# Kernel tuning notes

Hardware: AMD Instinct MI355X
Metric: run time of the kernel (lower is better)

Reference implementation:

```python
import jax, jax.numpy as jnp
import numpy as np

B, S, HID, H, D = 4, 1024, 1024, 16, 64
MAXP = 1024  # max_position_embeddings
EPS = 1e-8


def setup_inputs() -> dict:
    key = jax.random.key(0)
    ks = jax.random.split(key, 9)
    scale = 0.02  # keep logits small since masked_softmax has no max-subtraction
    return {
        "hidden_states": jax.random.normal(ks[0], (B, S, HID), jnp.float32),
        "attention_mask": jnp.zeros((B, 1, 1, S), jnp.float32),
        "skim_mask": jax.random.randint(ks[1], (B, S), 0, 2, jnp.int32),
        "Wq": jax.random.normal(ks[2], (HID, HID), jnp.float32) * scale,
        "bq": jnp.zeros((HID,), jnp.float32),
        "Wk": jax.random.normal(ks[3], (HID, HID), jnp.float32) * scale,
        "bk": jnp.zeros((HID,), jnp.float32),
        "Wv": jax.random.normal(ks[4], (HID, HID), jnp.float32) * scale,
        "bv": jnp.zeros((HID,), jnp.float32),
        "dist_emb": jax.random.normal(ks[5], (2 * MAXP - 1, D), jnp.float32) * scale,
    }


def reference(hidden_states, attention_mask, skim_mask, Wq, bq, Wk, bk, Wv, bv, dist_emb):
    # Linear projections (W stored as [in, out]) then split heads: [B,H,S,D]
    def heads(x):
        return x.reshape(B, S, H, D).transpose(0, 2, 1, 3)

    q = heads(hidden_states @ Wq + bq)
    k = heads(hidden_states @ Wk + bk)
    v = heads(hidden_states @ Wv + bv)

    # raw scores [B,H,S,S]
    scores = jnp.einsum('bhld,bhrd->bhlr', q, k)

    # relative_key positional bias
    pos = jnp.arange(S)
    distance = pos[:, None] - pos[None, :]                 # [S,S]
    pe = dist_emb[distance + MAXP - 1]                     # [S,S,D]
    scores = scores + jnp.einsum('bhld,lrd->bhlr', q, pe)

    scores = scores / jnp.sqrt(jnp.float32(D))
    scores = scores + attention_mask

    # skim_mask branch: masked_softmax (exp * mask, normalized with eps)
    mask = skim_mask[:, None, None, :].astype(scores.dtype)  # [B,1,1,S]
    exps = jnp.exp(scores) * mask
    probs = exps / (EPS + exps.sum(-1, keepdims=True))
    # dropout in eval mode -> identity

    ctx = jnp.einsum('bhlr,bhrd->bhld', probs, v)
    return ctx.transpose(0, 2, 1, 3).reshape(B, S, HID)
```

## Files before the change

### kernel.cpp

```cpp
#include <hip/hip_runtime.h>
#include <hip/hip_bf16.h>


#define EPSV 1e-8f

typedef short bfrag __attribute__((ext_vector_type(8)));
typedef float cfrag __attribute__((ext_vector_type(16)));

__device__ __forceinline__ short f2bf(float f) {
    __hip_bfloat16 h = __float2bfloat16(f);
    return *reinterpret_cast<short*>(&h);
}
__device__ __forceinline__ float bf2f(short s) {
    unsigned int u = ((unsigned int)(unsigned short)s) << 16;
    return __builtin_bit_cast(float, u);
}
__device__ __forceinline__ unsigned int pk2(short a, short b) {
    return (unsigned int)(unsigned short)a | ((unsigned int)(unsigned short)b << 16);
}

__global__ __launch_bounds__(256) void prep(
    const float* __restrict__ hidden, const float* __restrict__ Wq,
    const float* __restrict__ Wk, const float* __restrict__ Wv,
    const float* __restrict__ dist,
    short* __restrict__ Xs, short* __restrict__ Wt, short* __restrict__ Db)
{
    __shared__ short Tl[32 * 72];
    const int bid = blockIdx.x, tid = threadIdx.x;

    if (bid < 2048) {
        const int mt = bid >> 4, kg = bid & 15;
        const int m_l = tid >> 3, k8 = (tid & 7) * 8;
        const float* src = hidden + (size_t)(mt * 32 + m_l) * 1024 + kg * 64 + k8;
        float4 v0 = *(const float4*)src, v1 = *(const float4*)(src + 4);
        short o[8];
        o[0] = f2bf(v0.x); o[1] = f2bf(v0.y); o[2] = f2bf(v0.z); o[3] = f2bf(v0.w);
        o[4] = f2bf(v1.x); o[5] = f2bf(v1.y); o[6] = f2bf(v1.z); o[7] = f2bf(v1.w);
        *(bfrag*)&Tl[m_l * 72 + k8] = *(bfrag*)o;
        __syncthreads();
        const int l31 = tid & 31, q2 = (tid >> 5) & 1, kc = tid >> 6;
        bfrag r = *(const bfrag*)&Tl[l31 * 72 + kc * 16 + q2 * 8];
        *(bfrag*)(Xs + ((size_t)(mt * 64 + kg * 4 + kc) * 64 + q2 * 32 + l31) * 8) = r;
    } else if (bid < 3584) {
        const int t = bid - 2048, z = t >> 9, nt = (t >> 4) & 31, kg = t & 15;
        const float* W = (z == 0) ? Wq : ((z == 1) ? Wk : Wv);
        const int k_l = tid >> 2, n8 = (tid & 3) * 8;
        const float* src = W + (size_t)(kg * 64 + k_l) * 1024 + nt * 32 + n8;
        float4 v0 = *(const float4*)src, v1 = *(const float4*)(src + 4);
        float vv[8] = {v0.x, v0.y, v0.z, v0.w, v1.x, v1.y, v1.z, v1.w};
#pragma unroll
        for (int i = 0; i < 8; i++)
            Tl[(n8 + i) * 72 + k_l] = f2bf(vv[i]);
        __syncthreads();
        const int l31 = tid & 31, q2 = (tid >> 5) & 1, kc = tid >> 6;
        bfrag r = *(const bfrag*)&Tl[l31 * 72 + kc * 16 + q2 * 8];
        *(bfrag*)(Wt + (size_t)z * 1048576
                  + ((size_t)(nt * 64 + kg * 4 + kc) * 64 + q2 * 32 + l31) * 8) = r;
    } else {
        const int idx = (bid - 3584) * 256 + tid;
        if (idx < 16376) {
            const float* src = dist + (size_t)idx * 8;
            float4 v0 = *(const float4*)src, v1 = *(const float4*)(src + 4);
            short o[8];
            o[0] = f2bf(v0.x); o[1] = f2bf(v0.y); o[2] = f2bf(v0.z); o[3] = f2bf(v0.w);
            o[4] = f2bf(v1.x); o[5] = f2bf(v1.y); o[6] = f2bf(v1.z); o[7] = f2bf(v1.w);
            *(bfrag*)(Db + (size_t)idx * 8) = *(bfrag*)o;
        }
    }
}

__global__ __launch_bounds__(256) void qkv_mfma(
    const short* __restrict__ Xs, const short* __restrict__ Wt,
    const float* __restrict__ bq, const float* __restrict__ bk,
    const float* __restrict__ bv,
    short* __restrict__ Qf, short* __restrict__ Kf, short* __restrict__ Vt)
{
    const int z = blockIdx.z;
    const short* W = Wt + (size_t)z * 1048576;
    const float* bias = (z == 0) ? bq : ((z == 1) ? bk : bv);
    const float scale = (z == 0) ? 0.125f : 1.0f;

    const int tid = threadIdx.x, lane = tid & 63, wid = tid >> 6;
    const int q2 = lane >> 5, l31 = lane & 31;
    const int wr = wid >> 1, wc = wid & 1;
    const int m0 = blockIdx.x * 128, n0 = blockIdx.y * 128;

    cfrag acc[2][2];
#pragma unroll
    for (int i = 0; i < 2; i++)
#pragma unroll
        for (int j = 0; j < 2; j++)
#pragma unroll
            for (int e = 0; e < 16; e++) acc[i][j][e] = 0.f;

    const short* ap0 = Xs + ((size_t)((m0 >> 5) + wr * 2 + 0) * 64 * 64 + lane) * 8;
    const short* ap1 = Xs + ((size_t)((m0 >> 5) + wr * 2 + 1) * 64 * 64 + lane) * 8;
    const short* bp0 = W  + ((size_t)((n0 >> 5) + wc * 2 + 0) * 64 * 64 + lane) * 8;
    const short* bp1 = W  + ((size_t)((n0 >> 5) + wc * 2 + 1) * 64 * 64 + lane) * 8;

#pragma unroll 4
    for (int kc = 0; kc < 64; kc++) {
        const int off = kc * 512;
        bfrag a0 = *(const bfrag*)(ap0 + off);
        bfrag a1 = *(const bfrag*)(ap1 + off);
        bfrag b0 = *(const bfrag*)(bp0 + off);
        bfrag b1 = *(const bfrag*)(bp1 + off);
        acc[0][0] = __builtin_amdgcn_mfma_f32_32x32x16_bf16(a0, b0, acc[0][0], 0, 0, 0);
        acc[0][1] = __builtin_amdgcn_mfma_f32_32x32x16_bf16(a0, b1, acc[0][1], 0, 0, 0);
        acc[1][0] = __builtin_amdgcn_mfma_f32_32x32x16_bf16(a1, b0, acc[1][0], 0, 0, 0);
        acc[1][1] = __builtin_amdgcn_mfma_f32_32x32x16_bf16(a1, b1, acc[1][1], 0, 0, 0);
    }

#pragma unroll
    for (int nt = 0; nt < 2; nt++) {
        const int c = n0 + wc * 64 + nt * 32 + l31;
        const float bval = bias[c];
        const int h = c >> 6;
        const int d = nt * 32 + l31;
#pragma unroll
        for (int mt = 0; mt < 2; mt++) {
            const int tok0 = m0 + wr * 64 + mt * 32;
            const int bb = tok0 >> 10, s_base = tok0 & 1023;
            const size_t bhbase = (size_t)(bb * 16 + h) * 65536;
            if (z < 2) {
                short* outp = (z == 0) ? Qf : Kf;
                const size_t fbase = bhbase
                    + ((size_t)((s_base >> 5) * 4 + (d >> 4)) * 64
                       + ((d >> 3) & 1) * 32) * 8 + (d & 7);
#pragma unroll
                for (int reg = 0; reg < 16; reg++) {
                    const int row = (reg & 3) + 8 * (reg >> 2) + 4 * q2;
                    outp[fbase + (size_t)row * 8] = f2bf((acc[mt][nt][reg] + bval) * scale);
                }
            } else {
#pragma unroll
                for (int g = 0; g < 4; g++) {
                    const float e0 = acc[mt][nt][4 * g + 0] + bval;
                    const float e1 = acc[mt][nt][4 * g + 1] + bval;
                    const float e2 = acc[mt][nt][4 * g + 2] + bval;
                    const float e3 = acc[mt][nt][4 * g + 3] + bval;
                    uint2 w2;
                    w2.x = pk2(f2bf(e0), f2bf(e1));
                    w2.y = pk2(f2bf(e2), f2bf(e3));
                    const size_t flat = bhbase
                        + ((size_t)(nt * 64 + (s_base >> 4) + (g >> 1)) * 64
                           + (g & 1) * 32 + l31) * 8 + 4 * q2;
                    *(uint2*)(Vt + flat) = w2;
                }
            }
        }
    }
}

__global__ __launch_bounds__(256) void attn_mfma(
    const short* __restrict__ Qf, const short* __restrict__ Kf,
    const short* __restrict__ Vt, const short* __restrict__ Db,
    const float* __restrict__ amask, const int* __restrict__ skim,
    float* __restrict__ out)
{
    __shared__ short Tb[128 * 132];
    __shared__ short Es[4][32 * 72];
    __shared__ float Lg[1024];

    const int tid = threadIdx.x, lane = tid & 63, w = tid >> 6;
    const int q2 = lane >> 5, l31 = lane & 31;
    const int h2 = w >> 1;
    const int bh = blockIdx.x, b = bh >> 4, hh = bh & 15;
    const int l0 = blockIdx.y * 128;

    {
        const int r4 = tid * 4;
        float4 am = *(const float4*)(amask + b * 1024 + r4);
        int4 sk = *(const int4*)(skim + b * 1024 + r4);
        Lg[r4 + 0] = __expf(am.x) * (float)sk.x;
        Lg[r4 + 1] = __expf(am.y) * (float)sk.y;
        Lg[r4 + 2] = __expf(am.z) * (float)sk.z;
        Lg[r4 + 3] = __expf(am.w) * (float)sk.w;
    }
    __syncthreads();

    const short* Qg = Qf + (size_t)bh * 65536;
    const short* Kg = Kf + (size_t)bh * 65536;
    const short* Vg = Vt + (size_t)bh * 65536;

    bfrag qa[4];
#pragma unroll
    for (int c = 0; c < 4; c++)
        qa[c] = *(const bfrag*)(Qg + ((size_t)(((l0 >> 5) + w) * 4 + c) * 64 + lane) * 8);

    cfrag oacc[2];
#pragma unroll
    for (int mt = 0; mt < 2; mt++)
#pragma unroll
        for (int e = 0; e < 16; e++) oacc[mt][e] = 0.f;
    float esum = 0.f;

    const int lrow = 32 * w + l31;

    for (int r0 = -64; r0 < 1024; r0 += 64) {
        const int bd = l0 - r0 - 64 + 64 * h2;
#pragma unroll
        for (int mt = 0; mt < 2; mt++) {
            cfrag t;
#pragma unroll
            for (int e = 0; e < 16; e++) t[e] = 0.f;
            const int drow = bd + 32 * mt + l31;
            const int er = min(max(drow + 1023, 0), 2046);
#pragma unroll
            for (int kc = 0; kc < 4; kc++) {
                bfrag pb = *(const bfrag*)(Db + (size_t)er * 64 + kc * 16 + q2 * 8);
                t = __builtin_amdgcn_mfma_f32_32x32x16_bf16(pb, qa[kc], t, 0, 0, 0);
            }
#pragma unroll
            for (int g = 0; g < 4; g++) {
                const int slot = (bd + 32 * mt + 8 * g + 4 * q2) & 127;
                uint2 w2;
                w2.x = pk2(f2bf(t[4 * g + 0]), f2bf(t[4 * g + 1]));
                w2.y = pk2(f2bf(t[4 * g + 2]), f2bf(t[4 * g + 3]));
                *(uint2*)&Tb[lrow * 132 + slot] = w2;
            }
        }
        if (r0 < 0) continue;

        cfrag sfr[2];
#pragma unroll
        for (int mt = 0; mt < 2; mt++) {
#pragma unroll
            for (int e = 0; e < 16; e++) sfr[mt][e] = 0.f;
#pragma unroll
            for (int kc = 0; kc < 4; kc++) {
                bfrag kb = *(const bfrag*)(Kg
                    + ((size_t)(((r0 >> 5) + mt) * 4 + kc) * 64 + lane) * 8);
                sfr[mt] = __builtin_amdgcn_mfma_f32_32x32x16_bf16(
                    kb, qa[kc], sfr[mt], 0, 0, 0);
            }
        }

        const int lg = l0 + 32 * w + l31;
#pragma unroll
        for (int mt = 0; mt < 2; mt++) {
#pragma unroll
            for (int g = 0; g < 4; g++) {
                const int rb = r0 + 32 * mt + 8 * g + 4 * q2;
                float4 g4 = *(const float4*)&Lg[rb];
                short s4[4];
#pragma unroll
                for (int j = 0; j < 4; j++) {
                    const int dist = lg - (rb + j);
                    const float tv = bf2f(Tb[lrow * 132 + (dist & 127)]);
                    const float gv = (j == 0) ? g4.x : (j == 1) ? g4.y
                                   : (j == 2) ? g4.z : g4.w;
                    const float e = __expf(sfr[mt][4 * g + j] + tv) * gv;
                    s4[j] = f2bf(e);
                    esum += bf2f(s4[j]);
                }
                uint2 w2;
                w2.x = pk2(s4[0], s4[1]);
                w2.y = pk2(s4[2], s4[3]);
                *(uint2*)&Es[w][l31 * 72 + 32 * mt + 8 * g + 4 * q2] = w2;
            }
        }

#pragma unroll
        for (int kc = 0; kc < 4; kc++) {
            bfrag ef = *(const bfrag*)&Es[w][l31 * 72 + kc * 16 + q2 * 8];
#pragma unroll
            for (int mtd = 0; mtd < 2; mtd++) {
                bfrag vb = *(const bfrag*)(Vg
                    + ((size_t)(mtd * 64 + (r0 >> 4) + kc) * 64 + lane) * 8);
                oacc[mtd] = __builtin_amdgcn_mfma_f32_32x32x16_bf16(
                    vb, ef, oacc[mtd], 0, 0, 0);
            }
        }
    }

    const float den = EPSV + esum + __shfl_xor(esum, 32);
    const float inv = 1.0f / den;
    const int lg = l0 + 32 * w + l31;
    float* ob = out + ((size_t)(b * 1024 + lg) * 1024) + hh * 64;
#pragma unroll
    for (int mtd = 0; mtd < 2; mtd++) {
#pragma unroll
        for (int g = 0; g < 4; g++) {
            float4 o;
            o.x = oacc[mtd][4 * g + 0] * inv;
            o.y = oacc[mtd][4 * g + 1] * inv;
            o.z = oacc[mtd][4 * g + 2] * inv;
            o.w = oacc[mtd][4 * g + 3] * inv;
            *(float4*)(ob + 32 * mtd + 8 * g + 4 * q2) = o;
        }
    }
}

extern "C" void kernel_launch(void* const* d_in, const int* in_sizes, int n_in,
                              void* d_out, int out_size, void* d_ws, size_t ws_size,
                              hipStream_t stream) {
    const float* hidden = (const float*)d_in[0];
    const float* amask  = (const float*)d_in[1];
    const int*   skim   = (const int*)d_in[2];
    const float* Wq     = (const float*)d_in[3];
    const float* bq     = (const float*)d_in[4];
    const float* Wk     = (const float*)d_in[5];
    const float* bk     = (const float*)d_in[6];
    const float* Wv     = (const float*)d_in[7];
    const float* bv     = (const float*)d_in[8];
    const float* dist   = (const float*)d_in[9];
    float* out = (float*)d_out;

    char* w = (char*)d_ws;
    short* Xs  = (short*)(w);
    short* Wt  = (short*)(w + ((size_t)8 << 20));
    short* Db  = (short*)(w + ((size_t)14 << 20));
    short* Qf  = (short*)(w + ((size_t)15 << 20));
    short* Kf  = (short*)(w + ((size_t)23 << 20));
    short* Vt  = (short*)(w + ((size_t)31 << 20));

    prep<<<3648, 256, 0, stream>>>(hidden, Wq, Wk, Wv, dist, Xs, Wt, Db);
    qkv_mfma<<<dim3(32, 8, 3), 256, 0, stream>>>(Xs, Wt, bq, bk, bv, Qf, Kf, Vt);
    attn_mfma<<<dim3(64, 8), 256, 0, stream>>>(Qf, Kf, Vt, Db, amask, skim, out);
}
```

Baseline: 199.7 us.

## Split attention key range across two wave groups and pass probabilities via permlane

```diff
diff --git a/kernel.cpp b/kernel.cpp
--- a/kernel.cpp
+++ b/kernel.cpp
@@ -6,6 +6,7 @@
 
 typedef short bfrag __attribute__((ext_vector_type(8)));
 typedef float cfrag __attribute__((ext_vector_type(16)));
+typedef int v2i __attribute__((ext_vector_type(2)));
 
 __device__ __forceinline__ short f2bf(float f) {
     __hip_bfloat16 h = __float2bfloat16(f);
@@ -78,7 +79,7 @@
     const int z = blockIdx.z;
     const short* W = Wt + (size_t)z * 1048576;
     const float* bias = (z == 0) ? bq : ((z == 1) ? bk : bv);
-    const float scale = (z == 0) ? 0.125f : 1.0f;
+    const float scale = (z == 0) ? 0.18033688011112042f : 1.0f;
 
     const int tid = threadIdx.x, lane = tid & 63, wid = tid >> 6;
     const int q2 = lane >> 5, l31 = lane & 31;
@@ -152,30 +153,28 @@
     }
 }
 
-__global__ __launch_bounds__(256) void attn_mfma(
+__global__ __launch_bounds__(512, 4) void attn_mfma(
     const short* __restrict__ Qf, const short* __restrict__ Kf,
     const short* __restrict__ Vt, const short* __restrict__ Db,
     const float* __restrict__ amask, const int* __restrict__ skim,
     float* __restrict__ out)
 {
-    __shared__ short Tb[128 * 132];
-    __shared__ short Es[4][32 * 72];
+    __shared__ short Tb[256 * 130];
     __shared__ float Lg[1024];
 
     const int tid = threadIdx.x, lane = tid & 63, w = tid >> 6;
     const int q2 = lane >> 5, l31 = lane & 31;
-    const int h2 = w >> 1;
+    const int wl = w & 3, rh = w >> 2;
+    const int h2 = wl >> 1;
     const int bh = blockIdx.x, b = bh >> 4, hh = bh & 15;
     const int l0 = blockIdx.y * 128;
 
     {
-        const int r4 = tid * 4;
-        float4 am = *(const float4*)(amask + b * 1024 + r4);
-        int4 sk = *(const int4*)(skim + b * 1024 + r4);
-        Lg[r4 + 0] = __expf(am.x) * (float)sk.x;
-        Lg[r4 + 1] = __expf(am.y) * (float)sk.y;
-        Lg[r4 + 2] = __expf(am.z) * (float)sk.z;
-        Lg[r4 + 3] = __expf(am.w) * (float)sk.w;
+        const int r2 = tid * 2;
+        float2 am = *(const float2*)(amask + b * 1024 + r2);
+        int2 sk = *(const int2*)(skim + b * 1024 + r2);
+        Lg[r2 + 0] = __expf(am.x) * (float)sk.x;
+        Lg[r2 + 1] = __expf(am.y) * (float)sk.y;
     }
     __syncthreads();
 
@@ -186,18 +185,20 @@
     bfrag qa[4];
 #pragma unroll
     for (int c = 0; c < 4; c++)
-        qa[c] = *(const bfrag*)(Qg + ((size_t)(((l0 >> 5) + w) * 4 + c) * 64 + lane) * 8);
+        qa[c] = *(const bfrag*)(Qg + ((size_t)(((l0 >> 5) + wl) * 4 + c) * 64 + lane) * 8);
 
     cfrag oacc[2];
 #pragma unroll
     for (int mt = 0; mt < 2; mt++)
 #pragma unroll
         for (int e = 0; e < 16; e++) oacc[mt][e] = 0.f;
-    float esum = 0.f;
-
-    const int lrow = 32 * w + l31;
-
-    for (int r0 = -64; r0 < 1024; r0 += 64) {
+    float es[4] = {0.f, 0.f, 0.f, 0.f};
+
+    const int lrow130 = (32 * w + l31) * 130;
+    const int lg = l0 + 32 * wl + l31;
+    const int rbase = rh * 512;
+
+    for (int r0 = rbase - 64; r0 < rbase + 512; r0 += 64) {
         const int bd = l0 - r0 - 64 + 64 * h2;
 #pragma unroll
         for (int mt = 0; mt < 2; mt++) {
@@ -214,13 +215,13 @@
 #pragma unroll
             for (int g = 0; g < 4; g++) {
                 const int slot = (bd + 32 * mt + 8 * g + 4 * q2) & 127;
-                uint2 w2;
-                w2.x = pk2(f2bf(t[4 * g + 0]), f2bf(t[4 * g + 1]));
-                w2.y = pk2(f2bf(t[4 * g + 2]), f2bf(t[4 * g + 3]));
-                *(uint2*)&Tb[lrow * 132 + slot] = w2;
-            }
-        }
-        if (r0 < 0) continue;
+                *(unsigned int*)&Tb[lrow130 + slot] =
+                    pk2(f2bf(t[4 * g + 0]), f2bf(t[4 * g + 1]));
+                *(unsigned int*)&Tb[lrow130 + slot + 2] =
+                    pk2(f2bf(t[4 * g + 2]), f2bf(t[4 * g + 3]));
+            }
+        }
+        if (r0 < rbase) continue;
 
         cfrag sfr[2];
 #pragma unroll
@@ -236,58 +237,81 @@
             }
         }
 
-        const int lg = l0 + 32 * w + l31;
 #pragma unroll
         for (int mt = 0; mt < 2; mt++) {
+            unsigned int P[4][2];
 #pragma unroll
             for (int g = 0; g < 4; g++) {
                 const int rb = r0 + 32 * mt + 8 * g + 4 * q2;
                 float4 g4 = *(const float4*)&Lg[rb];
-                short s4[4];
+                float ev[4];
 #pragma unroll
                 for (int j = 0; j < 4; j++) {
                     const int dist = lg - (rb + j);
-                    const float tv = bf2f(Tb[lrow * 132 + (dist & 127)]);
+                    const float tv = bf2f(Tb[lrow130 + (dist & 127)]);
                     const float gv = (j == 0) ? g4.x : (j == 1) ? g4.y
                                    : (j == 2) ? g4.z : g4.w;
-                    const float e = __expf(sfr[mt][4 * g + j] + tv) * gv;
-                    s4[j] = f2bf(e);
-                    esum += bf2f(s4[j]);
+                    ev[j] = __builtin_amdgcn_exp2f(sfr[mt][4 * g + j] + tv) * gv;
+                    es[j] += ev[j];
                 }
-                uint2 w2;
-                w2.x = pk2(s4[0], s4[1]);
-                w2.y = pk2(s4[2], s4[3]);
-                *(uint2*)&Es[w][l31 * 72 + 32 * mt + 8 * g + 4 * q2] = w2;
-            }
-        }
-
-#pragma unroll
-        for (int kc = 0; kc < 4; kc++) {
-            bfrag ef = *(const bfrag*)&Es[w][l31 * 72 + kc * 16 + q2 * 8];
-#pragma unroll
-            for (int mtd = 0; mtd < 2; mtd++) {
-                bfrag vb = *(const bfrag*)(Vg
-                    + ((size_t)(mtd * 64 + (r0 >> 4) + kc) * 64 + lane) * 8);
-                oacc[mtd] = __builtin_amdgcn_mfma_f32_32x32x16_bf16(
-                    vb, ef, oacc[mtd], 0, 0, 0);
-            }
-        }
-    }
-
-    const float den = EPSV + esum + __shfl_xor(esum, 32);
-    const float inv = 1.0f / den;
-    const int lg = l0 + 32 * w + l31;
-    float* ob = out + ((size_t)(b * 1024 + lg) * 1024) + hh * 64;
-#pragma unroll
-    for (int mtd = 0; mtd < 2; mtd++) {
-#pragma unroll
-        for (int g = 0; g < 4; g++) {
-            float4 o;
-            o.x = oacc[mtd][4 * g + 0] * inv;
-            o.y = oacc[mtd][4 * g + 1] * inv;
-            o.z = oacc[mtd][4 * g + 2] * inv;
-            o.w = oacc[mtd][4 * g + 3] * inv;
-            *(float4*)(ob + 32 * mtd + 8 * g + 4 * q2) = o;
+                P[g][0] = pk2(f2bf(ev[0]), f2bf(ev[1]));
+                P[g][1] = pk2(f2bf(ev[2]), f2bf(ev[3]));
+            }
+#pragma unroll
+            for (int c = 0; c < 2; c++) {
+                v2i s0 = __builtin_amdgcn_permlane32_swap(
+                    (int)P[2 * c][0], (int)P[2 * c + 1][0], false, false);
+                v2i s1 = __builtin_amdgcn_permlane32_swap(
+                    (int)P[2 * c][1], (int)P[2 * c + 1][1], false, false);
+                union { bfrag f; int d[4]; } u;
+                u.d[0] = s0[0]; u.d[1] = s1[0]; u.d[2] = s0[1]; u.d[3] = s1[1];
+                const int kc = 2 * mt + c;
+#pragma unroll
+                for (int mtd = 0; mtd < 2; mtd++) {
+                    bfrag vb = *(const bfrag*)(Vg
+                        + ((size_t)(mtd * 64 + (r0 >> 4) + kc) * 64 + lane) * 8);
+                    oacc[mtd] = __builtin_amdgcn_mfma_f32_32x32x16_bf16(
+                        vb, u.f, oacc[mtd], 0, 0, 0);
+                }
+            }
+        }
+    }
+
+    float esum = (es[0] + es[1]) + (es[2] + es[3]);
+
+    __syncthreads();
+    float* Sb = (float*)Tb;
+    if (rh == 1) {
+#pragma unroll
+        for (int mtd = 0; mtd < 2; mtd++)
+#pragma unroll
+            for (int e = 0; e < 16; e++)
+                Sb[((mtd * 16 + e) * 4 + wl) * 64 + lane] = oacc[mtd][e];
+        Sb[8192 + wl * 64 + lane] = esum;
+    }
+    __syncthreads();
+    if (rh == 0) {
+#pragma unroll
+        for (int mtd = 0; mtd < 2; mtd++)
+#pragma unroll
+            for (int e = 0; e < 16; e++)
+                oacc[mtd][e] += Sb[((mtd * 16 + e) * 4 + wl) * 64 + lane];
+        esum += Sb[8192 + wl * 64 + lane];
+
+        const float den = EPSV + esum + __shfl_xor(esum, 32);
+        const float inv = 1.0f / den;
+        float* ob = out + ((size_t)(b * 1024 + lg) * 1024) + hh * 64;
+#pragma unroll
+        for (int mtd = 0; mtd < 2; mtd++) {
+#pragma unroll
+            for (int g = 0; g < 4; g++) {
+                float4 o;
+                o.x = oacc[mtd][4 * g + 0] * inv;
+                o.y = oacc[mtd][4 * g + 1] * inv;
+                o.z = oacc[mtd][4 * g + 2] * inv;
+                o.w = oacc[mtd][4 * g + 3] * inv;
+                *(float4*)(ob + 32 * mtd + 8 * g + 4 * q2) = o;
+            }
         }
     }
 }
@@ -317,5 +341,5 @@
 
     prep<<<3648, 256, 0, stream>>>(hidden, Wq, Wk, Wv, dist, Xs, Wt, Db);
     qkv_mfma<<<dim3(32, 8, 3), 256, 0, stream>>>(Xs, Wt, bq, bk, bv, Qf, Kf, Vt);
-    attn_mfma<<<dim3(64, 8), 256, 0, stream>>>(Qf, Kf, Vt, Db, amask, skim, out);
-}
+    attn_mfma<<<dim3(64, 8), 512, 0, stream>>>(Qf, Kf, Vt, Db, amask, skim, out);
+}
```

After: 234.6 us. 17.5% more time.

## Keep softmax probabilities in registers via permlane swap and fold log2e into Q

Applied to the files above, without the earlier changes.

```diff
diff --git a/kernel.cpp b/kernel.cpp
--- a/kernel.cpp
+++ b/kernel.cpp
@@ -6,6 +6,7 @@
 
 typedef short bfrag __attribute__((ext_vector_type(8)));
 typedef float cfrag __attribute__((ext_vector_type(16)));
+typedef int v2i __attribute__((ext_vector_type(2)));
 
 __device__ __forceinline__ short f2bf(float f) {
     __hip_bfloat16 h = __float2bfloat16(f);
@@ -78,7 +79,7 @@
     const int z = blockIdx.z;
     const short* W = Wt + (size_t)z * 1048576;
     const float* bias = (z == 0) ? bq : ((z == 1) ? bk : bv);
-    const float scale = (z == 0) ? 0.125f : 1.0f;
+    const float scale = (z == 0) ? 0.18033688011112042f : 1.0f;
 
     const int tid = threadIdx.x, lane = tid & 63, wid = tid >> 6;
     const int q2 = lane >> 5, l31 = lane & 31;
@@ -152,19 +153,17 @@
     }
 }
 
-__global__ __launch_bounds__(256) void attn_mfma(
+__global__ __launch_bounds__(256, 2) void attn_mfma(
     const short* __restrict__ Qf, const short* __restrict__ Kf,
     const short* __restrict__ Vt, const short* __restrict__ Db,
     const float* __restrict__ amask, const int* __restrict__ skim,
     float* __restrict__ out)
 {
     __shared__ short Tb[128 * 132];
-    __shared__ short Es[4][32 * 72];
     __shared__ float Lg[1024];
 
     const int tid = threadIdx.x, lane = tid & 63, w = tid >> 6;
     const int q2 = lane >> 5, l31 = lane & 31;
-    const int h2 = w >> 1;
     const int bh = blockIdx.x, b = bh >> 4, hh = bh & 15;
     const int l0 = blockIdx.y * 128;
 
@@ -193,90 +192,109 @@
     for (int mt = 0; mt < 2; mt++)
 #pragma unroll
         for (int e = 0; e < 16; e++) oacc[mt][e] = 0.f;
-    float esum = 0.f;
-
-    const int lrow = 32 * w + l31;
-
-    for (int r0 = -64; r0 < 1024; r0 += 64) {
-        const int bd = l0 - r0 - 64 + 64 * h2;
-#pragma unroll
-        for (int mt = 0; mt < 2; mt++) {
-            cfrag t;
-#pragma unroll
-            for (int e = 0; e < 16; e++) t[e] = 0.f;
-            const int drow = bd + 32 * mt + l31;
-            const int er = min(max(drow + 1023, 0), 2046);
-#pragma unroll
-            for (int kc = 0; kc < 4; kc++) {
-                bfrag pb = *(const bfrag*)(Db + (size_t)er * 64 + kc * 16 + q2 * 8);
-                t = __builtin_amdgcn_mfma_f32_32x32x16_bf16(pb, qa[kc], t, 0, 0, 0);
+    float es[4] = {0.f, 0.f, 0.f, 0.f};
+
+    const int Lband = l0 + 32 * w;
+    const int lg = Lband + l31;
+    const int rowb = (32 * w + l31) * 132;
+
+    for (int r0 = -128; r0 < 1024; r0 += 64) {
+        const bool produce = r0 < 960;
+
+        bfrag pb[2][4];
+        if (produce) {
+#pragma unroll
+            for (int mt = 0; mt < 2; mt++) {
+                const int D0 = Lband - r0 - 128 + 32 * mt;
+                const int er = min(max(D0 + l31 + 1023, 0), 2046);
+#pragma unroll
+                for (int kc = 0; kc < 4; kc++)
+                    pb[mt][kc] = *(const bfrag*)(Db + (size_t)er * 64 + kc * 16 + q2 * 8);
             }
-#pragma unroll
-            for (int g = 0; g < 4; g++) {
-                const int slot = (bd + 32 * mt + 8 * g + 4 * q2) & 127;
-                uint2 w2;
-                w2.x = pk2(f2bf(t[4 * g + 0]), f2bf(t[4 * g + 1]));
-                w2.y = pk2(f2bf(t[4 * g + 2]), f2bf(t[4 * g + 3]));
-                *(uint2*)&Tb[lrow * 132 + slot] = w2;
+        }
+
+        if (r0 >= 0) {
+            bfrag kb[2][4], vbl[4][2];
+#pragma unroll
+            for (int mt = 0; mt < 2; mt++)
+#pragma unroll
+                for (int kc = 0; kc < 4; kc++)
+                    kb[mt][kc] = *(const bfrag*)(Kg
+                        + ((size_t)(((r0 >> 5) + mt) * 4 + kc) * 64 + lane) * 8);
+#pragma unroll
+            for (int kc = 0; kc < 4; kc++)
+#pragma unroll
+                for (int mtd = 0; mtd < 2; mtd++)
+                    vbl[kc][mtd] = *(const bfrag*)(Vg
+                        + ((size_t)(mtd * 64 + (r0 >> 4) + kc) * 64 + lane) * 8);
+
+#pragma unroll
+            for (int mt = 0; mt < 2; mt++) {
+                cfrag sfr;
+#pragma unroll
+                for (int e = 0; e < 16; e++) sfr[e] = 0.f;
+#pragma unroll
+                for (int kc = 0; kc < 4; kc++)
+                    sfr = __builtin_amdgcn_mfma_f32_32x32x16_bf16(
+                        kb[mt][kc], qa[kc], sfr, 0, 0, 0);
+
+                unsigned int P[4][2];
+#pragma unroll
+                for (int g = 0; g < 4; g++) {
+                    const int rb = r0 + 32 * mt + 8 * g + 4 * q2;
+                    float4 g4 = *(const float4*)&Lg[rb];
+                    v2i tr = *(const v2i*)&Tb[rowb + (rb & 127)];
+                    const float tv0 = __builtin_bit_cast(float, (unsigned)tr[0] << 16);
+                    const float tv1 = __builtin_bit_cast(float, (unsigned)tr[0] & 0xffff0000u);
+                    const float tv2 = __builtin_bit_cast(float, (unsigned)tr[1] << 16);
+                    const float tv3 = __builtin_bit_cast(float, (unsigned)tr[1] & 0xffff0000u);
+                    float ev0 = __builtin_amdgcn_exp2f(sfr[4 * g + 0] + tv0) * g4.x;
+                    float ev1 = __builtin_amdgcn_exp2f(sfr[4 * g + 1] + tv1) * g4.y;
+                    float ev2 = __builtin_amdgcn_exp2f(sfr[4 * g + 2] + tv2) * g4.z;
+                    float ev3 = __builtin_amdgcn_exp2f(sfr[4 * g + 3] + tv3) * g4.w;
+                    es[0] += ev0; es[1] += ev1; es[2] += ev2; es[3] += ev3;
+                    P[g][0] = pk2(f2bf(ev0), f2bf(ev1));
+                    P[g][1] = pk2(f2bf(ev2), f2bf(ev3));
+                }
+#pragma unroll
+                for (int c = 0; c < 2; c++) {
+                    v2i s0 = __builtin_amdgcn_permlane32_swap(
+                        (int)P[2 * c][0], (int)P[2 * c + 1][0], false, false);
+                    v2i s1 = __builtin_amdgcn_permlane32_swap(
+                        (int)P[2 * c][1], (int)P[2 * c + 1][1], false, false);
+                    union { bfrag f; int d[4]; } u;
+                    u.d[0] = s0[0]; u.d[1] = s1[0]; u.d[2] = s0[1]; u.d[3] = s1[1];
+                    const int kc = 2 * mt + c;
+#pragma unroll
+                    for (int mtd = 0; mtd < 2; mtd++)
+                        oacc[mtd] = __builtin_amdgcn_mfma_f32_32x32x16_bf16(
+                            vbl[kc][mtd], u.f, oacc[mtd], 0, 0, 0);
+                }
             }
         }
-        if (r0 < 0) continue;
-
-        cfrag sfr[2];
-#pragma unroll
-        for (int mt = 0; mt < 2; mt++) {
-#pragma unroll
-            for (int e = 0; e < 16; e++) sfr[mt][e] = 0.f;
-#pragma unroll
-            for (int kc = 0; kc < 4; kc++) {
-                bfrag kb = *(const bfrag*)(Kg
-                    + ((size_t)(((r0 >> 5) + mt) * 4 + kc) * 64 + lane) * 8);
-                sfr[mt] = __builtin_amdgcn_mfma_f32_32x32x16_bf16(
-                    kb, qa[kc], sfr[mt], 0, 0, 0);
+
+        if (produce) {
+#pragma unroll
+            for (int mt = 0; mt < 2; mt++) {
+                cfrag t;
+#pragma unroll
+                for (int e = 0; e < 16; e++) t[e] = 0.f;
+#pragma unroll
+                for (int kc = 0; kc < 4; kc++)
+                    t = __builtin_amdgcn_mfma_f32_32x32x16_bf16(
+                        pb[mt][kc], qa[kc], t, 0, 0, 0);
+#pragma unroll
+                for (int e = 0; e < 16; e++) {
+                    const int rr = (e & 3) + 8 * (e >> 2) + 4 * q2;
+                    Tb[rowb + ((l31 + r0 - 32 * mt - rr) & 127)] = f2bf(t[e]);
+                }
             }
         }
-
-        const int lg = l0 + 32 * w + l31;
-#pragma unroll
-        for (int mt = 0; mt < 2; mt++) {
-#pragma unroll
-            for (int g = 0; g < 4; g++) {
-                const int rb = r0 + 32 * mt + 8 * g + 4 * q2;
-                float4 g4 = *(const float4*)&Lg[rb];
-                short s4[4];
-#pragma unroll
-                for (int j = 0; j < 4; j++) {
-                    const int dist = lg - (rb + j);
-                    const float tv = bf2f(Tb[lrow * 132 + (dist & 127)]);
-                    const float gv = (j == 0) ? g4.x : (j == 1) ? g4.y
-                                   : (j == 2) ? g4.z : g4.w;
-                    const float e = __expf(sfr[mt][4 * g + j] + tv) * gv;
-                    s4[j] = f2bf(e);
-                    esum += bf2f(s4[j]);
-                }
-                uint2 w2;
-                w2.x = pk2(s4[0], s4[1]);
-                w2.y = pk2(s4[2], s4[3]);
-                *(uint2*)&Es[w][l31 * 72 + 32 * mt + 8 * g + 4 * q2] = w2;
-            }
-        }
-
-#pragma unroll
-        for (int kc = 0; kc < 4; kc++) {
-            bfrag ef = *(const bfrag*)&Es[w][l31 * 72 + kc * 16 + q2 * 8];
-#pragma unroll
-            for (int mtd = 0; mtd < 2; mtd++) {
-                bfrag vb = *(const bfrag*)(Vg
-                    + ((size_t)(mtd * 64 + (r0 >> 4) + kc) * 64 + lane) * 8);
-                oacc[mtd] = __builtin_amdgcn_mfma_f32_32x32x16_bf16(
-                    vb, ef, oacc[mtd], 0, 0, 0);
-            }
-        }
-    }
-
+    }
+
+    float esum = (es[0] + es[1]) + (es[2] + es[3]);
     const float den = EPSV + esum + __shfl_xor(esum, 32);
     const float inv = 1.0f / den;
-    const int lg = l0 + 32 * w + l31;
     float* ob = out + ((size_t)(b * 1024 + lg) * 1024) + hh * 64;
 #pragma unroll
     for (int mtd = 0; mtd < 2; mtd++) {
```

New measurement: 196.2 us. No clear change (-1.8%).
